# Optimization experiments

Measured on AMD Instinct MI355X. Metric: run time of the kernel, lower is better.

The kernel has to match this reference:

```python
import jax, jax.numpy as jnp
import numpy as np

B, S, HID = 2, 2048, 2048
H, KV, D = 16, 8, 128          # heads, kv heads, head_dim
GROUPS = H // KV               # 2
RATIO = 0.5
SCALING = D ** -0.5
MIN = float(np.finfo(np.float32).min)


def rotate_half(x):
    x1, x2 = x[..., : D // 2], x[..., D // 2 :]
    return jnp.concatenate((-x2, x1), axis=-1)


def setup_inputs() -> dict:
    key = jax.random.key(0)
    ks = jax.random.split(key, 9)
    hidden_states = jax.random.normal(ks[0], (B, S, HID), jnp.float32)
    # rotary tables (bounded like real cos/sin)
    cos = jax.random.uniform(ks[1], (B, S, D), jnp.float32)
    sin = jax.random.uniform(ks[2], (B, S, D), jnp.float32)
    # additive causal mask [B,1,S,S]: 0 where allowed, finfo.min above diagonal
    causal = jnp.triu(jnp.ones((S, S), bool), k=1)
    attention_mask = jnp.where(causal, MIN, 0.0).astype(jnp.float32)[None, None]
    attention_mask = jnp.broadcast_to(attention_mask, (B, 1, S, S))
    sd = 1.0 / np.sqrt(HID)
    Wq = jax.random.normal(ks[3], (H * D, HID), jnp.float32) * sd
    Wk = jax.random.normal(ks[4], (KV * D, HID), jnp.float32) * sd
    Wv = jax.random.normal(ks[5], (KV * D, HID), jnp.float32) * sd
    A = jax.random.normal(ks[6], (H,), jnp.float32) * 0.1
    Wdt = jax.random.normal(ks[7], (H, KV * D), jnp.float32) * (1.0 / np.sqrt(KV * D))
    Wo = jax.random.normal(ks[8], (HID, H * D), jnp.float32) * (1.0 / np.sqrt(H * D))
    return {"hidden_states": hidden_states, "cos": cos, "sin": sin,
            "attention_mask": attention_mask, "Wq": Wq, "Wk": Wk, "Wv": Wv,
            "A": A, "Wdt": Wdt, "Wo": Wo}


def reference(hidden_states, cos, sin, attention_mask, Wq, Wk, Wv, A, Wdt, Wo):
    x = hidden_states
    # fused QKV projections -> [B, heads, S, D]
    q = (x @ Wq.T).reshape(B, S, H, D).transpose(0, 2, 1, 3)
    k = (x @ Wk.T).reshape(B, S, KV, D).transpose(0, 2, 1, 3)
    v = (x @ Wv.T).reshape(B, S, KV, D).transpose(0, 2, 1, 3)
    # RoPE (cos/sin unsqueezed on head dim)
    c, s = cos[:, None], sin[:, None]
    q = q * c + rotate_half(q) * s
    k = k * c + rotate_half(k) * s
    # dynamic mask: dt_proj(value) -> softplus -> exp, per head  [B, H, S]
    v_flat = v.transpose(0, 2, 1, 3).reshape(B, S, KV * D)
    dt = v_flat @ Wdt.T                                    # [B,S,H]
    dyn = jnp.exp(A * jax.nn.softplus(dt)).transpose(0, 2, 1)  # [B,H,S]
    # kthvalue thresholding (k-th smallest along keys)
    num_dyn = int(S * RATIO)                               # 1024
    kth = jnp.sort(dyn, axis=-1)[..., num_dyn - 1 : num_dyn]   # [B,H,1]
    attn_mask = jnp.where(dyn < kth, MIN, dyn)[:, :, None, :]  # [B,H,1,S]
    attn_mask = attn_mask + attention_mask                 # [B,H,S,S]
    # GQA repeat kv
    k_rep = jnp.repeat(k, GROUPS, axis=1)
    v_rep = jnp.repeat(v, GROUPS, axis=1)
    scores = jnp.einsum("bhqd,bhkd->bhqk", q, k_rep) * SCALING + attn_mask
    w = jax.nn.softmax(scores.astype(jnp.float32), axis=-1).astype(q.dtype)
    out = jnp.einsum("bhqk,bhkd->bhqd", w, v_rep)
    out = out.transpose(0, 2, 1, 3).reshape(B, S, H * D)
    return out @ Wo.T
```

## Files before the change

kernel.cpp:

```cpp
#include <hip/hip_runtime.h>

typedef unsigned short u16;
typedef _Float16 f16x8 __attribute__((ext_vector_type(8)));
typedef float f32x4 __attribute__((ext_vector_type(4)));
typedef u16 u16x8 __attribute__((ext_vector_type(8)));

#define MINF (-0x1.fffffep+127f)
#define SCALE 0.08838834764831845f

__device__ __forceinline__ u16 f2h(float f) {
    _Float16 h = (_Float16)f;
    return __builtin_bit_cast(u16, h);
}
__device__ __forceinline__ float h2f(u16 u) {
    _Float16 h = __builtin_bit_cast(_Float16, u);
    return (float)h;
}

typedef const __attribute__((address_space(1))) void* gptr_t;
typedef __attribute__((address_space(3))) void* sptr_t;
#define GLDS16(g, l) __builtin_amdgcn_global_load_lds((gptr_t)(const void*)(g), (sptr_t)(void*)(l), 16, 0, 0)

__global__ void convk8(const float* __restrict__ in, u16* __restrict__ out, int n) {
    int i = (blockIdx.x * 256 + threadIdx.x) * 8;
    if (i >= n) return;
    f32x4 a = *(const f32x4*)&in[i];
    f32x4 b = *(const f32x4*)&in[i + 4];
    u16x8 r;
#pragma unroll
    for (int j = 0; j < 4; ++j) { r[j] = f2h(a[j]); r[j + 4] = f2h(b[j]); }
    *(u16x8*)&out[i] = r;
}

__global__ __launch_bounds__(512, 1) void gemm8_qkv(
    const u16* __restrict__ A, const u16* __restrict__ Bw,
    u16* __restrict__ qo, u16* __restrict__ ko, u16* __restrict__ vto) {
    __shared__ alignas(16) u16 AS[2][2][128 * 64];
    __shared__ alignas(16) u16 BS[2][2][128 * 64];
    const int K = 2048, NT = 32;
    int tid = threadIdx.x;
    int wid = tid >> 6, lane = tid & 63;
    int l16 = lane & 15, lhi = lane >> 4;
    int wm = wid >> 2, wn = wid & 3;
    int bm = blockIdx.y * 256, bn = blockIdx.x * 256;
    int srow = lane >> 3;
    int schunk = (lane & 7) ^ srow;
    f32x4 acc[8][4] = {};

    auto STAGE = [&](int t, int buf) {
        int kt = t * 64;
#pragma unroll
        for (int i = 0; i < 2; ++i) {
            int c = wid * 2 + i;
            int row = c * 8 + srow;
            const u16* sa0 = A + (size_t)(bm + row) * K + kt + schunk * 8;
            GLDS16(sa0, &AS[buf][0][c * 512]);
            const u16* sa1 = A + (size_t)(bm + 128 + row) * K + kt + schunk * 8;
            GLDS16(sa1, &AS[buf][1][c * 512]);
            const u16* sb0 = Bw + (size_t)(bn + row) * K + kt + schunk * 8;
            GLDS16(sb0, &BS[buf][0][c * 512]);
            const u16* sb1 = Bw + (size_t)(bn + 128 + row) * K + kt + schunk * 8;
            GLDS16(sb1, &BS[buf][1][c * 512]);
        }
    };

    auto COMPUTE = [&](int buf) {
#pragma unroll
        for (int kk = 0; kk < 2; ++kk) {
            f16x8 af[8], bf[4];
#pragma unroll
            for (int ni = 0; ni < 4; ++ni) {
                int rb = wn * 64 + ni * 16 + l16;
                int half = rb >> 7, rh = rb & 127;
                int c2 = (kk * 4 + lhi) ^ (rh & 7);
                bf[ni] = *(const f16x8*)&BS[buf][half][rh * 64 + c2 * 8];
            }
#pragma unroll
            for (int mi = 0; mi < 8; ++mi) {
                int rh = mi * 16 + l16;
                int c2 = (kk * 4 + lhi) ^ (rh & 7);
                af[mi] = *(const f16x8*)&AS[buf][wm][rh * 64 + c2 * 8];
            }
            __builtin_amdgcn_s_setprio(1);
#pragma unroll
            for (int mi = 0; mi < 8; ++mi)
#pragma unroll
                for (int ni = 0; ni < 4; ++ni)
                    acc[mi][ni] = __builtin_amdgcn_mfma_f32_16x16x32_f16(af[mi], bf[ni], acc[mi][ni], 0, 0, 0);
            __builtin_amdgcn_s_setprio(0);
        }
    };

    STAGE(0, 0);
    STAGE(1, 1);
    asm volatile("s_waitcnt vmcnt(8)" ::: "memory");
    __builtin_amdgcn_sched_barrier(0);
    __builtin_amdgcn_s_barrier();

    for (int t = 0; t < NT; ++t) {
        int buf = t & 1;
        COMPUTE(buf);
        __builtin_amdgcn_s_barrier();
        if (t + 2 < NT) {
            STAGE(t + 2, buf);
            asm volatile("s_waitcnt vmcnt(8)" ::: "memory");
        } else {
            asm volatile("s_waitcnt vmcnt(0)" ::: "memory");
        }
        __builtin_amdgcn_sched_barrier(0);
        __builtin_amdgcn_s_barrier();
    }

#pragma unroll
    for (int mi = 0; mi < 8; ++mi) {
#pragma unroll
        for (int ni = 0; ni < 4; ++ni) {
#pragma unroll
            for (int j = 0; j < 4; ++j) {
                int r = bm + wm * 128 + mi * 16 + lhi * 4 + j;
                int c = bn + wn * 64 + ni * 16 + l16;
                u16 hv = f2h(acc[mi][ni][j]);
                int b = r >> 11, s = r & 2047;
                if (c < 2048) {
                    int hh = c >> 7, d = c & 127;
                    qo[(((size_t)(b * 16 + hh)) * 2048 + s) * 128 + d] = hv;
                } else if (c < 3072) {
                    int hh = (c - 2048) >> 7, d = c & 127;
                    ko[(((size_t)(b * 8 + hh)) * 2048 + s) * 128 + d] = hv;
                } else {
                    int hh = (c - 3072) >> 7, d = c & 127;
                    vto[(((size_t)(b * 8 + hh)) * 128 + d) * 2048 + s] = hv;
                }
            }
        }
    }
}

__global__ __launch_bounds__(256) void gemm_bt0(
    const u16* __restrict__ A, const u16* __restrict__ Bw, float* __restrict__ Cf, int N, int K) {
    __shared__ alignas(16) u16 As[128 * 32];
    __shared__ alignas(16) u16 Bs[128 * 32];
    int tid = threadIdx.x;
    int wid = tid >> 6, lane = tid & 63;
    int l16 = lane & 15, lhi = lane >> 4;
    int bm = blockIdx.y * 128, bn = blockIdx.x * 128;
    int wr = (wid >> 1) * 64, wc = (wid & 1) * 64;
    int srow = lane >> 2, sseg = lane & 3;
    f32x4 acc[4][4] = {};
    for (int kt = 0; kt < K; kt += 32) {
        __syncthreads();
#pragma unroll
        for (int i = 0; i < 2; ++i) {
            const u16* ga = A + (size_t)(bm + i * 64 + wid * 16 + srow) * K + kt + sseg * 8;
            GLDS16(ga, &As[(i * 64 + wid * 16) * 32]);
            const u16* gb = Bw + (size_t)(bn + i * 64 + wid * 16 + srow) * K + kt + sseg * 8;
            GLDS16(gb, &Bs[(i * 64 + wid * 16) * 32]);
        }
        __syncthreads();
        f16x8 af[4], bf[4];
#pragma unroll
        for (int mi = 0; mi < 4; ++mi) af[mi] = *(const f16x8*)&As[(wr + mi * 16 + l16) * 32 + lhi * 8];
#pragma unroll
        for (int ni = 0; ni < 4; ++ni) bf[ni] = *(const f16x8*)&Bs[(wc + ni * 16 + l16) * 32 + lhi * 8];
#pragma unroll
        for (int mi = 0; mi < 4; ++mi)
#pragma unroll
            for (int ni = 0; ni < 4; ++ni)
                acc[mi][ni] = __builtin_amdgcn_mfma_f32_16x16x32_f16(af[mi], bf[ni], acc[mi][ni], 0, 0, 0);
    }
#pragma unroll
    for (int mi = 0; mi < 4; ++mi)
#pragma unroll
        for (int ni = 0; ni < 4; ++ni)
#pragma unroll
            for (int j = 0; j < 4; ++j) {
                int r = bm + wr + mi * 16 + lhi * 4 + j;
                int c = bn + wc + ni * 16 + l16;
                Cf[(size_t)r * N + c] = acc[mi][ni][j];
            }
}

__global__ void rope_kernel(u16* __restrict__ t, const float* __restrict__ cosv,
                            const float* __restrict__ sinv, int nheads) {
    int i = blockIdx.x * 256 + threadIdx.x;
    int total = 2 * nheads * 2048 * 64;
    if (i >= total) return;
    int d = i & 63;
    int s = (i >> 6) & 2047;
    int bh = i >> 17;
    int b = bh / nheads;
    size_t base = ((size_t)bh * 2048 + s) * 128;
    size_t cb = ((size_t)b * 2048 + s) * 128;
    float x1 = h2f(t[base + d]), x2 = h2f(t[base + d + 64]);
    float c1 = cosv[cb + d], s1 = sinv[cb + d];
    float c2 = cosv[cb + d + 64], s2 = sinv[cb + d + 64];
    t[base + d] = f2h(x1 * c1 - x2 * s1);
    t[base + d + 64] = f2h(x2 * c2 + x1 * s2);
}

__global__ void wdtv_kernel(const float* __restrict__ Wdt, const float* __restrict__ Wv,
                            float* __restrict__ out) {
    int t = threadIdx.x;
    int h = blockIdx.x >> 3;
    int c = (blockIdx.x & 7) * 256 + t;
    const float* wd = Wdt + h * 1024;
    float acc = 0.f;
    for (int f = 0; f < 1024; ++f) acc += wd[f] * Wv[(size_t)f * 2048 + c];
    out[h * 2048 + c] = acc;
}

__global__ void dt_dyn_kernel(const float* __restrict__ x, const float* __restrict__ Wdtv,
                              const float* __restrict__ Av, float* __restrict__ dyn) {
    __shared__ float xrow[2048];
    __shared__ float red[256];
    int bs = blockIdx.x;
    int t = threadIdx.x;
    for (int i = t; i < 2048; i += 256) xrow[i] = x[(size_t)bs * 2048 + i];
    __syncthreads();
    int h = t & 15, chunk = t >> 4;
    float p = 0.f;
    const float* wrow = Wdtv + h * 2048 + chunk * 128;
    const float* xr = xrow + chunk * 128;
    for (int f = 0; f < 128; ++f) p += xr[f] * wrow[f];
    red[t] = p;
    __syncthreads();
    if (t < 16) {
        float dt = 0.f;
        for (int c = 0; c < 16; ++c) dt += red[c * 16 + t];
        float sp = fmaxf(dt, 0.f) + log1pf(expf(-fabsf(dt)));
        int b = bs >> 11, s = bs & 2047;
        dyn[((size_t)(b * 16 + t)) * 2048 + s] = expf(Av[t] * sp);
    }
}

__global__ void kth_mask_kernel(const float* __restrict__ dyn, float* __restrict__ mval) {
    __shared__ float sv[2048];
    int bh = blockIdx.x, t = threadIdx.x;
    const float* row = dyn + (size_t)bh * 2048;
    sv[t] = row[t];
    sv[t + 1024] = row[t + 1024];
    __syncthreads();
    for (int k = 2; k <= 2048; k <<= 1) {
        for (int j = k >> 1; j > 0; j >>= 1) {
#pragma unroll 1
            for (int base = 0; base < 2048; base += 1024) {
                int i = base + t;
                int ixj = i ^ j;
                if (ixj > i) {
                    float a = sv[i], b = sv[ixj];
                    bool up = ((i & k) == 0);
                    if ((a > b) == up) { sv[i] = b; sv[ixj] = a; }
                }
            }
            __syncthreads();
        }
    }
    float kth = sv[1023];
    float v0 = row[t];
    float v1 = row[t + 1024];
    mval[(size_t)bh * 2048 + t] = v0 < kth ? MINF : v0;
    mval[(size_t)bh * 2048 + t + 1024] = v1 < kth ? MINF : v1;
}

__global__ __launch_bounds__(256) void attn_kernel(
    const u16* __restrict__ qb, const u16* __restrict__ kb, const u16* __restrict__ vtb,
    const float* __restrict__ mv, u16* __restrict__ ao) {
    __shared__ alignas(16) u16 Kst[2][64 * 128];
    __shared__ alignas(16) u16 Vst[2][128 * 64];
    __shared__ alignas(16) u16 plds[4][16 * 72];
    __shared__ int flags[4];
    int bh = blockIdx.x;
    int qt = 31 - blockIdx.y;
    int b = bh >> 4, h = bh & 15, kvh = h >> 1;
    int wid = threadIdx.x >> 6, lane = threadIdx.x & 63;
    int l16 = lane & 15, lhi = lane >> 4;
    int q0 = qt * 64 + wid * 16;
    const u16* qbase = qb + (((size_t)bh * 2048) + q0) * 128;
    const u16* kbase = kb + ((size_t)(b * 8 + kvh) * 2048) * 128;
    const u16* vtbase = vtb + ((size_t)(b * 8 + kvh) * 128) * 2048;
    const float* mvb = mv + (size_t)bh * 2048;
    u16* pw = plds[wid];
    int rx = l16 & 7;

    auto STAGE = [&](int kt2, int bidx) {
        int kvb2 = kt2 * 64;
#pragma unroll
        for (int i = 0; i < 4; ++i) {
            int call = wid * 4 + i;
            int r = call * 4 + (lane >> 4);
            int gch = (lane & 15) ^ (r & 7);
            const u16* src = kbase + (size_t)(kvb2 + r) * 128 + gch * 8;
            GLDS16(src, &Kst[bidx][call * 512]);
        }
#pragma unroll
        for (int i = 0; i < 4; ++i) {
            int call = wid * 4 + i;
            int d = call * 8 + (lane >> 3);
            int gch = (lane & 7) ^ (d & 7);
            const u16* src = vtbase + (size_t)d * 2048 + kvb2 + gch * 8;
            GLDS16(src, &Vst[bidx][call * 512]);
        }
    };

    f16x8 qf[4];
#pragma unroll
    for (int kc = 0; kc < 4; ++kc) qf[kc] = *(const f16x8*)&qbase[l16 * 128 + kc * 32 + lhi * 8];
    f16x8 ones;
#pragma unroll
    for (int i = 0; i < 8; ++i) ones[i] = (_Float16)1.f;
    float m[4];
#pragma unroll
    for (int j = 0; j < 4; ++j) m[j] = -INFINITY;
    f32x4 accO[8] = {};
    f32x4 accS = {};

    STAGE(0, 0);
    __syncthreads();

    for (int kt = 0; kt < 32; ++kt) {
        if (kt > qt) {
            if (!(flags[0] | flags[1] | flags[2] | flags[3])) break;
        }
        int buf = kt & 1;
        if (kt + 1 < 32) STAGE(kt + 1, buf ^ 1);
        int kvb = kt * 64;

        f32x4 sc[4] = {};
#pragma unroll
        for (int ni = 0; ni < 4; ++ni) {
            const u16* kr = &Kst[buf][(ni * 16 + l16) * 128];
#pragma unroll
            for (int kc = 0; kc < 4; ++kc) {
                int cc = (kc * 4 + lhi) ^ rx;
                f16x8 kf = *(const f16x8*)&kr[cc * 8];
                sc[ni] = __builtin_amdgcn_mfma_f32_16x16x32_f16(qf[kc], kf, sc[ni], 0, 0, 0);
            }
        }

        float rmax[4] = {-INFINITY, -INFINITY, -INFINITY, -INFINITY};
#pragma unroll
        for (int ni = 0; ni < 4; ++ni) {
            int key = kvb + ni * 16 + l16;
            float mk = mvb[key];
#pragma unroll
            for (int j = 0; j < 4; ++j) {
                int qrow = q0 + lhi * 4 + j;
                float sval = sc[ni][j] * SCALE + (mk + (key > qrow ? MINF : 0.f));
                sc[ni][j] = sval;
                rmax[j] = fmaxf(rmax[j], sval);
            }
        }
#pragma unroll
        for (int j = 0; j < 4; ++j) {
#pragma unroll
            for (int off = 1; off < 16; off <<= 1) rmax[j] = fmaxf(rmax[j], __shfl_xor(rmax[j], off));
        }
        float mn[4];
        bool need = false;
#pragma unroll
        for (int j = 0; j < 4; ++j) {
            mn[j] = fmaxf(m[j], rmax[j]);
            need |= (mn[j] - m[j] > 8.0f);
        }
        if (__any(need)) {
#pragma unroll
            for (int j = 0; j < 4; ++j) {
                float r = __expf(m[j] - mn[j]);
                m[j] = mn[j];
                accS[j] *= r;
#pragma unroll
                for (int db = 0; db < 8; ++db) accO[db][j] *= r;
            }
        }
#pragma unroll
        for (int ni = 0; ni < 4; ++ni) {
#pragma unroll
            for (int j = 0; j < 4; ++j) {
                float pv = __expf(sc[ni][j] - m[j]);
                pw[(lhi * 4 + j) * 72 + ni * 16 + l16] = f2h(pv);
            }
        }

#pragma unroll
        for (int kc2 = 0; kc2 < 2; ++kc2) {
            f16x8 pa = *(const f16x8*)&pw[l16 * 72 + kc2 * 32 + lhi * 8];
            accS = __builtin_amdgcn_mfma_f32_16x16x32_f16(pa, ones, accS, 0, 0, 0);
#pragma unroll
            for (int db = 0; db < 8; ++db) {
                int cc = (kc2 * 4 + lhi) ^ rx;
                f16x8 vf = *(const f16x8*)&Vst[buf][(db * 16 + l16) * 64 + cc * 8];
                accO[db] = __builtin_amdgcn_mfma_f32_16x16x32_f16(pa, vf, accO[db], 0, 0, 0);
            }
        }

        bool deg = (m[0] == MINF) | (m[1] == MINF) | (m[2] == MINF) | (m[3] == MINF);
        if (lane == 0) flags[wid] = __any(deg) ? 1 : 0;
        __syncthreads();
    }

#pragma unroll
    for (int db = 0; db < 8; ++db) {
#pragma unroll
        for (int j = 0; j < 4; ++j) {
            int qrow = q0 + lhi * 4 + j;
            int d = db * 16 + l16;
            float o = accO[db][j] / accS[j];
            ao[((size_t)(b * 2048) + qrow) * 2048 + h * 128 + d] = f2h(o);
        }
    }
}

extern "C" void kernel_launch(void* const* d_in, const int* in_sizes, int n_in,
                              void* d_out, int out_size, void* d_ws, size_t ws_size,
                              hipStream_t stream) {
    const float* x = (const float*)d_in[0];
    const float* cosv = (const float*)d_in[1];
    const float* sinv = (const float*)d_in[2];
    const float* Wq = (const float*)d_in[4];
    const float* Wk = (const float*)d_in[5];
    const float* Wv = (const float*)d_in[6];
    const float* Av = (const float*)d_in[7];
    const float* Wdt = (const float*)d_in[8];
    const float* Wo = (const float*)d_in[9];

    char* ws = (char*)d_ws;
    u16* qb = (u16*)(ws);
    u16* kb = (u16*)(ws + 16777216);
    u16* vtb = (u16*)(ws + 25165824);
    float* dyn = (float*)(ws + 33554432);
    float* mval = (float*)(ws + 33816576);
    float* wdtv = (float*)(ws + 34078720);
    u16* xbf = (u16*)(ws + 34209792);
    u16* wbf = (u16*)(ws + 50987008);

    convk8<<<8388608 / 2048, 256, 0, stream>>>(x, xbf, 8388608);
    convk8<<<4194304 / 2048, 256, 0, stream>>>(Wq, wbf, 4194304);
    convk8<<<2097152 / 2048, 256, 0, stream>>>(Wk, wbf + 4194304, 2097152);
    convk8<<<2097152 / 2048, 256, 0, stream>>>(Wv, wbf + 6291456, 2097152);

    dim3 g1(16, 16);
    gemm8_qkv<<<g1, 512, 0, stream>>>(xbf, wbf, qb, kb, vtb);

    rope_kernel<<<16384, 256, 0, stream>>>(qb, cosv, sinv, 16);
    rope_kernel<<<8192, 256, 0, stream>>>(kb, cosv, sinv, 8);

    wdtv_kernel<<<128, 256, 0, stream>>>(Wdt, Wv, wdtv);
    dt_dyn_kernel<<<4096, 256, 0, stream>>>(x, wdtv, Av, dyn);
    kth_mask_kernel<<<32, 1024, 0, stream>>>(dyn, mval);

    convk8<<<4194304 / 2048, 256, 0, stream>>>(Wo, wbf, 4194304);

    dim3 g2(32, 32);
    attn_kernel<<<g2, 256, 0, stream>>>(qb, kb, vtb, mval, xbf);

    dim3 g3(16, 32);
    gemm_bt0<<<g3, 256, 0, stream>>>(xbf, wbf, (float*)d_out, 2048, 2048);
}
```

Measured before the change: 463.1 us.

## Replace output GEMM with double-buffered swizzled 256x128 kernel and fuse RoPE launches

The output projection GEMM moves from a 128x128 tile with single-buffered K=32 steps to a 256x128 tile with 8 waves. It uses K=64 steps, double-buffered LDS filled by async global-to-LDS loads, an XOR-swizzled LDS layout and MFMA priority hints, so loads overlap compute and LDS bank conflicts drop. The two RoPE launches become one kernel that loads cos/sin once per position and applies them across all q and k heads. The risks are lower occupancy (launch bounds 512,1 with large LDS) and fewer blocks for the output GEMM (256 vs 512).

```diff
diff --git a/kernel.cpp b/kernel.cpp
--- a/kernel.cpp
+++ b/kernel.cpp
@@ -136,66 +136,116 @@
     }
 }
 
-__global__ __launch_bounds__(256) void gemm_bt0(
-    const u16* __restrict__ A, const u16* __restrict__ Bw, float* __restrict__ Cf, int N, int K) {
-    __shared__ alignas(16) u16 As[128 * 32];
-    __shared__ alignas(16) u16 Bs[128 * 32];
+__global__ __launch_bounds__(512, 1) void gemm8_op(
+    const u16* __restrict__ A, const u16* __restrict__ Bw, float* __restrict__ Cf) {
+    __shared__ alignas(16) u16 AS[2][2][128 * 64];
+    __shared__ alignas(16) u16 BS[2][128 * 64];
+    const int K = 2048, NT = 32;
     int tid = threadIdx.x;
     int wid = tid >> 6, lane = tid & 63;
     int l16 = lane & 15, lhi = lane >> 4;
-    int bm = blockIdx.y * 128, bn = blockIdx.x * 128;
-    int wr = (wid >> 1) * 64, wc = (wid & 1) * 64;
-    int srow = lane >> 2, sseg = lane & 3;
-    f32x4 acc[4][4] = {};
-    for (int kt = 0; kt < K; kt += 32) {
-        __syncthreads();
+    int wm = wid >> 2, wn = wid & 3;
+    int bm = blockIdx.y * 256, bn = blockIdx.x * 128;
+    int srow = lane >> 3;
+    int schunk = (lane & 7) ^ srow;
+    f32x4 acc[8][2] = {};
+
+    auto STAGE = [&](int t, int buf) {
+        int kt = t * 64;
 #pragma unroll
         for (int i = 0; i < 2; ++i) {
-            const u16* ga = A + (size_t)(bm + i * 64 + wid * 16 + srow) * K + kt + sseg * 8;
-            GLDS16(ga, &As[(i * 64 + wid * 16) * 32]);
-            const u16* gb = Bw + (size_t)(bn + i * 64 + wid * 16 + srow) * K + kt + sseg * 8;
-            GLDS16(gb, &Bs[(i * 64 + wid * 16) * 32]);
-        }
-        __syncthreads();
-        f16x8 af[4], bf[4];
-#pragma unroll
-        for (int mi = 0; mi < 4; ++mi) af[mi] = *(const f16x8*)&As[(wr + mi * 16 + l16) * 32 + lhi * 8];
-#pragma unroll
-        for (int ni = 0; ni < 4; ++ni) bf[ni] = *(const f16x8*)&Bs[(wc + ni * 16 + l16) * 32 + lhi * 8];
-#pragma unroll
-        for (int mi = 0; mi < 4; ++mi)
-#pragma unroll
-            for (int ni = 0; ni < 4; ++ni)
-                acc[mi][ni] = __builtin_amdgcn_mfma_f32_16x16x32_f16(af[mi], bf[ni], acc[mi][ni], 0, 0, 0);
-    }
-#pragma unroll
-    for (int mi = 0; mi < 4; ++mi)
-#pragma unroll
-        for (int ni = 0; ni < 4; ++ni)
+            int c = wid * 2 + i;
+            int row = c * 8 + srow;
+            const u16* sa0 = A + (size_t)(bm + row) * K + kt + schunk * 8;
+            GLDS16(sa0, &AS[buf][0][c * 512]);
+            const u16* sa1 = A + (size_t)(bm + 128 + row) * K + kt + schunk * 8;
+            GLDS16(sa1, &AS[buf][1][c * 512]);
+            const u16* sb0 = Bw + (size_t)(bn + row) * K + kt + schunk * 8;
+            GLDS16(sb0, &BS[buf][c * 512]);
+        }
+    };
+
+    auto COMPUTE = [&](int buf) {
+#pragma unroll
+        for (int kk = 0; kk < 2; ++kk) {
+            f16x8 af[8], bf[2];
+#pragma unroll
+            for (int ni = 0; ni < 2; ++ni) {
+                int rb = wn * 32 + ni * 16 + l16;
+                int c2 = (kk * 4 + lhi) ^ (rb & 7);
+                bf[ni] = *(const f16x8*)&BS[buf][rb * 64 + c2 * 8];
+            }
+#pragma unroll
+            for (int mi = 0; mi < 8; ++mi) {
+                int rh = mi * 16 + l16;
+                int c2 = (kk * 4 + lhi) ^ (rh & 7);
+                af[mi] = *(const f16x8*)&AS[buf][wm][rh * 64 + c2 * 8];
+            }
+            __builtin_amdgcn_s_setprio(1);
+#pragma unroll
+            for (int mi = 0; mi < 8; ++mi)
+#pragma unroll
+                for (int ni = 0; ni < 2; ++ni)
+                    acc[mi][ni] = __builtin_amdgcn_mfma_f32_16x16x32_f16(af[mi], bf[ni], acc[mi][ni], 0, 0, 0);
+            __builtin_amdgcn_s_setprio(0);
+        }
+    };
+
+    STAGE(0, 0);
+    STAGE(1, 1);
+    asm volatile("s_waitcnt vmcnt(6)" ::: "memory");
+    __builtin_amdgcn_sched_barrier(0);
+    __builtin_amdgcn_s_barrier();
+
+    for (int t = 0; t < NT; ++t) {
+        int buf = t & 1;
+        COMPUTE(buf);
+        __builtin_amdgcn_s_barrier();
+        if (t + 2 < NT) {
+            STAGE(t + 2, buf);
+            asm volatile("s_waitcnt vmcnt(6)" ::: "memory");
+        } else {
+            asm volatile("s_waitcnt vmcnt(0)" ::: "memory");
+        }
+        __builtin_amdgcn_sched_barrier(0);
+        __builtin_amdgcn_s_barrier();
+    }
+
+#pragma unroll
+    for (int mi = 0; mi < 8; ++mi)
+#pragma unroll
+        for (int ni = 0; ni < 2; ++ni)
 #pragma unroll
             for (int j = 0; j < 4; ++j) {
-                int r = bm + wr + mi * 16 + lhi * 4 + j;
-                int c = bn + wc + ni * 16 + l16;
-                Cf[(size_t)r * N + c] = acc[mi][ni][j];
-            }
-}
-
-__global__ void rope_kernel(u16* __restrict__ t, const float* __restrict__ cosv,
-                            const float* __restrict__ sinv, int nheads) {
+                int r = bm + wm * 128 + mi * 16 + lhi * 4 + j;
+                int c = bn + wn * 32 + ni * 16 + l16;
+                Cf[(size_t)r * 2048 + c] = acc[mi][ni][j];
+            }
+}
+
+__global__ void rope_fused(u16* __restrict__ q, u16* __restrict__ k,
+                           const float* __restrict__ cosv, const float* __restrict__ sinv) {
     int i = blockIdx.x * 256 + threadIdx.x;
-    int total = 2 * nheads * 2048 * 64;
-    if (i >= total) return;
     int d = i & 63;
     int s = (i >> 6) & 2047;
-    int bh = i >> 17;
-    int b = bh / nheads;
-    size_t base = ((size_t)bh * 2048 + s) * 128;
+    int b = i >> 17;
     size_t cb = ((size_t)b * 2048 + s) * 128;
-    float x1 = h2f(t[base + d]), x2 = h2f(t[base + d + 64]);
     float c1 = cosv[cb + d], s1 = sinv[cb + d];
     float c2 = cosv[cb + d + 64], s2 = sinv[cb + d + 64];
-    t[base + d] = f2h(x1 * c1 - x2 * s1);
-    t[base + d + 64] = f2h(x2 * c2 + x1 * s2);
+#pragma unroll
+    for (int h = 0; h < 16; ++h) {
+        size_t base = (((size_t)(b * 16 + h)) * 2048 + s) * 128;
+        float x1 = h2f(q[base + d]), x2 = h2f(q[base + d + 64]);
+        q[base + d] = f2h(x1 * c1 - x2 * s1);
+        q[base + d + 64] = f2h(x2 * c2 + x1 * s2);
+    }
+#pragma unroll
+    for (int h = 0; h < 8; ++h) {
+        size_t base = (((size_t)(b * 8 + h)) * 2048 + s) * 128;
+        float x1 = h2f(k[base + d]), x2 = h2f(k[base + d + 64]);
+        k[base + d] = f2h(x1 * c1 - x2 * s1);
+        k[base + d + 64] = f2h(x2 * c2 + x1 * s2);
+    }
 }
 
 __global__ void wdtv_kernel(const float* __restrict__ Wdt, const float* __restrict__ Wv,
@@ -441,8 +491,7 @@
     dim3 g1(16, 16);
     gemm8_qkv<<<g1, 512, 0, stream>>>(xbf, wbf, qb, kb, vtb);
 
-    rope_kernel<<<16384, 256, 0, stream>>>(qb, cosv, sinv, 16);
-    rope_kernel<<<8192, 256, 0, stream>>>(kb, cosv, sinv, 8);
+    rope_fused<<<1024, 256, 0, stream>>>(qb, kb, cosv, sinv);
 
     wdtv_kernel<<<128, 256, 0, stream>>>(Wdt, Wv, wdtv);
     dt_dyn_kernel<<<4096, 256, 0, stream>>>(x, wdtv, Av, dyn);
@@ -453,6 +502,6 @@
     dim3 g2(32, 32);
     attn_kernel<<<g2, 256, 0, stream>>>(qb, kb, vtb, mval, xbf);
 
-    dim3 g3(16, 32);
-    gemm_bt0<<<g3, 256, 0, stream>>>(xbf, wbf, (float*)d_out, 2048, 2048);
-}
+    dim3 g3(16, 16);
+    gemm8_op<<<g3, 512, 0, stream>>>(xbf, wbf, (float*)d_out);
+}
```

New measurement: 446.7 us. -3.5%, faster.
